# Optimization experiments

Hardware: AMD Instinct MI355X
Metric: run time of the kernel (lower is better)

## Reference

```python
import jax, jax.numpy as jnp
import numpy as np

PAD = 0
SOS = 1
NEG = -1e9


def _lstm_scan(x, Wih, Whh, b, h0, c0, reverse=False):
    # x: [T, B, in]; torch gate order i, f, g, o
    def step(carry, xt):
        h, c = carry
        g = xt @ Wih.T + h @ Whh.T + b
        i, f, gg, o = jnp.split(g, 4, axis=-1)
        c = jax.nn.sigmoid(f) * c + jax.nn.sigmoid(i) * jnp.tanh(gg)
        h = jax.nn.sigmoid(o) * jnp.tanh(c)
        return (h, c), h
    (hT, cT), hs = jax.lax.scan(step, (h0, c0), x, reverse=reverse)
    return hs, hT, cT


def setup_inputs() -> dict:
    B, Ts, Tt = 32, 64, 66
    E, H, V = 512, 512, 16000
    key = jax.random.key(0)
    ks = jax.random.split(key, 16)
    s = 0.05
    n = lambda k, shape: (jax.random.normal(k, shape, dtype=jnp.float32) * s)
    return {
        'src_sentences': jax.random.randint(ks[0], (B, Ts), 4, V),
        'trg_sentences': jax.random.randint(ks[1], (B, Tt), 4, V),
        'src_emb': n(ks[2], (V, E)),
        'trg_emb': n(ks[3], (V, E)),
        'enc0_Wih': n(ks[4], (2, 4 * H, E)),
        'enc0_Whh': n(ks[5], (2, 4 * H, H)),
        'enc0_b': n(ks[6], (2, 4 * H)),
        'enc1_Wih': n(ks[7], (2, 4 * H, 2 * H)),
        'enc1_Whh': n(ks[8], (2, 4 * H, H)),
        'enc1_b': n(ks[9], (2, 4 * H)),
        'dec_Wih': n(ks[10], (8 * H, E)),      # LSTMCell: hidden = 2H -> 4*(2H) gates
        'dec_Whh': n(ks[11], (8 * H, 2 * H)),
        'dec_b': n(ks[12], (8 * H)),
        'out_W1': n(ks[13], (H, 4 * H)),
        'out_W2': n(ks[14], (V - 4, H)),
    }


def reference(src_sentences, trg_sentences, src_emb, trg_emb,
              enc0_Wih, enc0_Whh, enc0_b, enc1_Wih, enc1_Whh, enc1_b,
              dec_Wih, dec_Whh, dec_b, out_W1, out_W2):
    B, Ts = src_sentences.shape
    Tt = trg_sentences.shape[1]
    H = out_W1.shape[0]
    dt = src_emb.dtype
    enc_mask = src_sentences == PAD            # [B, Ts] (all False here)

    # ---- encoder: 2-layer bidirectional LSTM (dropout inactive / eval) ----
    x = jnp.swapaxes(src_emb[src_sentences], 0, 1)   # [Ts, B, E]
    z = jnp.zeros((B, H), dt)
    hf0, hfT, cfT = _lstm_scan(x, enc0_Wih[0], enc0_Whh[0], enc0_b[0], z, z)
    hb0, hbT, cbT = _lstm_scan(x, enc0_Wih[1], enc0_Whh[1], enc0_b[1], z, z, reverse=True)
    x1 = jnp.concatenate([hf0, hb0], axis=-1)        # [Ts, B, 2H]
    hf1, _, _ = _lstm_scan(x1, enc1_Wih[0], enc1_Whh[0], enc1_b[0], z, z)
    hb1, _, _ = _lstm_scan(x1, enc1_Wih[1], enc1_Whh[1], enc1_b[1], z, z, reverse=True)
    enc_out = jnp.swapaxes(jnp.concatenate([hf1, hb1], axis=-1), 0, 1)  # [B, Ts, 2H]
    # module uses encoder_hidden_t[0], [1] -> layer-0 fwd/bwd final states
    hidden = jnp.concatenate([hfT, hbT], axis=-1)    # [B, 2H]
    cell = jnp.concatenate([cfT, cbT], axis=-1)

    # ---- decoder: teacher_force = 1.0 (deterministic) ----
    steps = Tt - 2
    emb_in = jnp.swapaxes(trg_emb[trg_sentences[:, :steps]], 0, 1)  # [steps, B, E]
    tgts = jnp.swapaxes(trg_sentences[:, 1:steps + 1], 0, 1)        # [steps, B]

    def step(carry, inp):
        h, c, loss = carry
        xt, tgt = inp
        g = xt @ dec_Wih.T + h @ dec_Whh.T + dec_b
        i, f, gg, o = jnp.split(g, 4, axis=-1)
        c = jax.nn.sigmoid(f) * c + jax.nn.sigmoid(i) * jnp.tanh(gg)
        h = jax.nn.sigmoid(o) * jnp.tanh(c)
        dmask = tgt == PAD
        h = jnp.where(dmask[:, None], jnp.zeros((), dt), h)  # decoder_hidden_t[mask] = 0
        # dot attention over encoder states
        scores = jnp.einsum('btd,bd->bt', enc_out, h)
        scores = jnp.where(enc_mask, NEG, scores)
        attn = jax.nn.softmax(scores, axis=1)
        ctx = jnp.einsum('bt,btd->bd', attn, enc_out)
        zt = jnp.tanh(jnp.concatenate([h, ctx], axis=-1) @ out_W1.T)
        logits = zt @ out_W2.T                                # [B, V-4]
        logp = jax.nn.log_softmax(logits, axis=1)
        tgt_idx = tgt - 4
        valid = tgt_idx != -4                                 # ignore_index=-4 (PAD)
        safe = jnp.where(valid, tgt_idx, 0)
        nll = -jnp.take_along_axis(logp, safe[:, None], axis=1)[:, 0]
        loss = loss + jnp.sum(jnp.where(valid, nll, jnp.zeros((), dt)))
        pred = jnp.argmax(logits, axis=1) + 4
        return (h, c, loss), pred

    (_, _, loss), preds = jax.lax.scan(step, (hidden, cell, jnp.zeros((), dt)), (emb_in, tgts))
    denom = jnp.sum(trg_sentences[:, 1:-1] != PAD).astype(dt)
    return loss / denom, preds.T  # preds: [B, steps]
```

## Files before the change

### kernel.cpp

```cpp
#include <hip/hip_runtime.h>
#include <hip/hip_bf16.h>
#include <math.h>

#define TSRC 64
#define TTRG 66
#define NVOC 15996
#define NTILE 125

__device__ __forceinline__ float sigm(float x){ return 1.f/(1.f+expf(-x)); }

__global__ __launch_bounds__(256)
void k_gemm128(const float* __restrict__ A, int lda,
               const float* __restrict__ Bw, int ldb,
               const float* __restrict__ bias,
               float* __restrict__ C, int ldc, int K, int nNb)
{
  const int tid = threadIdx.x;
  const int mb = blockIdx.x / nNb;
  const int nb = blockIdx.x % nNb;
  const int m0 = mb*128, n0 = nb*128;

  __shared__ alignas(16) float As[16][132];
  __shared__ alignas(16) float Bs[16][132];
  const int tx = tid & 15;
  const int ty = tid >> 4;
  float acc[8][8];
  #pragma unroll
  for (int i=0;i<8;i++)
    #pragma unroll
    for (int j=0;j<8;j++) acc[i][j]=0.f;

  for (int kt=0; kt<K; kt+=16) {
    #pragma unroll
    for (int i=tid; i<128*16; i+=256) {
      int m = i>>4, k = i&15;
      As[k][m] = A[(size_t)(m0+m)*lda + kt + k];
    }
    #pragma unroll
    for (int i=tid; i<128*16; i+=256) {
      int n = i>>4, k = i&15;
      Bs[k][n] = Bw[(size_t)(n0+n)*ldb + kt + k];
    }
    __syncthreads();
    #pragma unroll
    for (int k=0;k<16;k++) {
      float4 a0 = *reinterpret_cast<const float4*>(&As[k][ty*4]);
      float4 a1 = *reinterpret_cast<const float4*>(&As[k][64+ty*4]);
      float4 b0 = *reinterpret_cast<const float4*>(&Bs[k][tx*4]);
      float4 b1 = *reinterpret_cast<const float4*>(&Bs[k][64+tx*4]);
      float av[8] = {a0.x,a0.y,a0.z,a0.w,a1.x,a1.y,a1.z,a1.w};
      float bv[8] = {b0.x,b0.y,b0.z,b0.w,b1.x,b1.y,b1.z,b1.w};
      #pragma unroll
      for (int i=0;i<8;i++)
        #pragma unroll
        for (int j=0;j<8;j++)
          acc[i][j] = fmaf(av[i], bv[j], acc[i][j]);
    }
    __syncthreads();
  }
  #pragma unroll
  for (int i=0;i<8;i++) {
    int m = m0 + ((i<4) ? ty*4+i : 64+ty*4+(i-4));
    int nA = n0 + tx*4, nB = n0 + 64 + tx*4;
    float4 v0, v1;
    v0.x = acc[i][0] + (bias?bias[nA+0]:0.f);
    v0.y = acc[i][1] + (bias?bias[nA+1]:0.f);
    v0.z = acc[i][2] + (bias?bias[nA+2]:0.f);
    v0.w = acc[i][3] + (bias?bias[nA+3]:0.f);
    v1.x = acc[i][4] + (bias?bias[nB+0]:0.f);
    v1.y = acc[i][5] + (bias?bias[nB+1]:0.f);
    v1.z = acc[i][6] + (bias?bias[nB+2]:0.f);
    v1.w = acc[i][7] + (bias?bias[nB+3]:0.f);
    *reinterpret_cast<float4*>(&C[(size_t)m*ldc + nA]) = v0;
    *reinterpret_cast<float4*>(&C[(size_t)m*ldc + nB]) = v1;
  }
}

__global__ __launch_bounds__(256)
void k_logits(const float* __restrict__ A, const float* __restrict__ Bw,
              const int* __restrict__ trg,
              float* __restrict__ Pmax, int* __restrict__ Parg,
              float* __restrict__ Psum, float* __restrict__ Ltgt)
{
  const int tid = threadIdx.x;
  const int j8   = blockIdx.x & 7;
  const int mb   = (blockIdx.x >> 3) & 15;
  const int nb   = ((blockIdx.x >> 7) << 3) + j8;
  if (nb >= NTILE) return;
  const int m0 = mb*128, n0 = nb*128;

  __shared__ alignas(16) float As[16][132];
  __shared__ alignas(16) float Bs[16][132];
  const int tx = tid & 15;
  const int ty = tid >> 4;
  float acc[8][8];
  #pragma unroll
  for (int i=0;i<8;i++)
    #pragma unroll
    for (int j=0;j<8;j++) acc[i][j]=0.f;

  for (int kt=0; kt<512; kt+=16) {
    #pragma unroll
    for (int i=tid; i<128*16; i+=256) {
      int m = i>>4, k = i&15;
      As[k][m] = A[(size_t)(m0+m)*512 + kt + k];
    }
    #pragma unroll
    for (int i=tid; i<128*16; i+=256) {
      int n = i>>4, k = i&15;
      int gn = n0+n;
      Bs[k][n] = (gn < NVOC) ? Bw[(size_t)gn*512 + kt + k] : 0.f;
    }
    __syncthreads();
    #pragma unroll
    for (int k=0;k<16;k++) {
      float4 a0 = *reinterpret_cast<const float4*>(&As[k][ty*4]);
      float4 a1 = *reinterpret_cast<const float4*>(&As[k][64+ty*4]);
      float4 b0 = *reinterpret_cast<const float4*>(&Bs[k][tx*4]);
      float4 b1 = *reinterpret_cast<const float4*>(&Bs[k][64+tx*4]);
      float av[8] = {a0.x,a0.y,a0.z,a0.w,a1.x,a1.y,a1.z,a1.w};
      float bv[8] = {b0.x,b0.y,b0.z,b0.w,b1.x,b1.y,b1.z,b1.w};
      #pragma unroll
      for (int i=0;i<8;i++)
        #pragma unroll
        for (int j=0;j<8;j++)
          acc[i][j] = fmaf(av[i], bv[j], acc[i][j]);
    }
    __syncthreads();
  }

  #pragma unroll
  for (int i=0;i<8;i++) {
    int r = m0 + ((i<4) ? ty*4+i : 64+ty*4+(i-4));
    int step = r >> 5, b = r & 31;
    int tgt = trg[b*TTRG + step + 1];
    int ti = tgt - 4;
    float m = -3.4e38f; int am = 0x7fffffff;
    #pragma unroll
    for (int j=0;j<8;j++) {
      int gn = n0 + ((j<4) ? tx*4+j : 64+tx*4+(j-4));
      if (gn < NVOC) {
        float x = acc[i][j];
        if (x > m || (x == m && gn < am)) { m = x; am = gn; }
      }
    }
    float s = 0.f;
    float lt = 0.f;
    #pragma unroll
    for (int j=0;j<8;j++) {
      int gn = n0 + ((j<4) ? tx*4+j : 64+tx*4+(j-4));
      if (gn < NVOC) {
        s += expf(acc[i][j] - m);
        if (gn == ti) lt = acc[i][j];
      }
    }
    #pragma unroll
    for (int d=1; d<16; d<<=1) {
      float m2 = __shfl_xor(m, d);
      int   a2 = __shfl_xor(am, d);
      float s2 = __shfl_xor(s, d);
      float l2 = __shfl_xor(lt, d);
      float M = fmaxf(m, m2);
      s = s*expf(m - M) + s2*expf(m2 - M);
      if (m2 > m || (m2 == m && a2 < am)) am = a2;
      m = M;
      lt += l2;
    }
    if (tx == 0) {
      size_t pi = (size_t)r*NTILE + nb;
      Pmax[pi] = m; Parg[pi] = am; Psum[pi] = s;
      if (ti >= n0 && ti < n0 + 128) Ltgt[r] = lt;
    }
  }
}

struct GArgs {
  const float* A;  int lda;
  const float* Bw; int ldb;
  const float* bias;
  float* C; int ldc;
  int N; int K; int nNb; int act;
};

template<int BM,int BN,int BK,int TM,int TN>
__global__ __launch_bounds__(256)
void k_gemm(GArgs a)
{
  const int tid = threadIdx.x;
  const int mb = blockIdx.x / a.nNb;
  const int nb = blockIdx.x % a.nNb;
  const int m0 = mb*BM, n0 = nb*BN;
  const float* A  = a.A + (size_t)m0*a.lda;
  const float* Bw = a.Bw;

  __shared__ float As[BK][BM+1];
  __shared__ float Bs[BK][BN+4];
  const int tx = tid % (BN/TN);
  const int ty = tid / (BN/TN);
  float acc[TM][TN];
  #pragma unroll
  for (int i=0;i<TM;i++)
    #pragma unroll
    for (int j=0;j<TN;j++) acc[i][j]=0.f;

  for (int kt=0; kt<a.K; kt+=BK) {
    #pragma unroll
    for (int i=tid; i<BM*BK; i+=256) {
      int m = i/BK, k = i%BK;
      As[k][m] = A[(size_t)m*a.lda + kt + k];
    }
    #pragma unroll
    for (int i=tid; i<BN*BK; i+=256) {
      int n = i/BK, k = i%BK;
      int gn = n0+n;
      Bs[k][n] = (gn < a.N) ? Bw[(size_t)gn*a.ldb + kt + k] : 0.f;
    }
    __syncthreads();
    #pragma unroll
    for (int k=0;k<BK;k++) {
      float av[TM], bv[TN];
      #pragma unroll
      for (int i=0;i<TM;i++) av[i]=As[k][ty*TM+i];
      #pragma unroll
      for (int j=0;j<TN;j++) bv[j]=Bs[k][tx*TN+j];
      #pragma unroll
      for (int i=0;i<TM;i++)
        #pragma unroll
        for (int j=0;j<TN;j++)
          acc[i][j] = fmaf(av[i], bv[j], acc[i][j]);
    }
    __syncthreads();
  }
  #pragma unroll
  for (int i=0;i<TM;i++) {
    int m = m0 + ty*TM + i;
    #pragma unroll
    for (int j=0;j<TN;j++) {
      int n = n0 + tx*TN + j;
      if (n < a.N) {
        float v = acc[i][j];
        if (a.bias) v += a.bias[n];
        if (a.act)  v = tanhf(v);
        a.C[(size_t)m*a.ldc + n] = v;
      }
    }
  }
}

__global__ __launch_bounds__(128)
void k_combine(const float* __restrict__ Pmax, const int* __restrict__ Parg,
               const float* __restrict__ Psum, const float* __restrict__ Ltgt,
               const int* __restrict__ trg,
               float* __restrict__ nll, float* __restrict__ outp)
{
  int r = blockIdx.x;
  int step = r >> 5, b = r & 31;
  int tid = threadIdx.x;
  __shared__ float sm[128]; __shared__ int sa[128]; __shared__ float ssum[128];
  float m = -3.4e38f; int am = 0x7fffffff; float s = 0.f;
  if (tid < NTILE) {
    size_t pi = (size_t)r*NTILE + tid;
    m = Pmax[pi]; am = Parg[pi]; s = Psum[pi];
  }
  sm[tid]=m; sa[tid]=am; ssum[tid]=s; __syncthreads();
  for (int off=64; off; off>>=1) {
    if (tid < off) {
      float m2 = sm[tid+off]; int a2 = sa[tid+off]; float s2 = ssum[tid+off];
      float m1 = sm[tid];     int a1 = sa[tid];     float s1 = ssum[tid];
      float M = fmaxf(m1, m2);
      ssum[tid] = s1*expf(m1 - M) + s2*expf(m2 - M);
      if (m2 > m1 || (m2 == m1 && a2 < a1)) sa[tid] = a2;
      sm[tid] = M;
    }
    __syncthreads();
  }
  if (tid == 0) {
    int tgt = trg[b*TTRG + step + 1];
    float nl = 0.f;
    if (tgt != 0) nl = -(Ltgt[r] - sm[0] - logf(ssum[0]));
    nll[step*32 + b] = nl;
    outp[1 + b*64 + step] = (float)(sa[0] + 4);
  }
}

__global__ void k_gather(const float* __restrict__ emb, const int* __restrict__ tok,
                         float* __restrict__ outp, int Tfull)
{
  int r = blockIdx.x;
  int t = r >> 5, b = r & 31;
  int token = tok[b*Tfull + t];
  const float4* s = (const float4*)(emb + (size_t)token*512);
  float4* d = (float4*)(outp + (size_t)r*512);
  d[threadIdx.x] = s[threadIdx.x];
}

__global__ __launch_bounds__(256)
void k_estep(const float* __restrict__ Whh,
             const float* __restrict__ xg,
             const float* __restrict__ hin,
             float* __restrict__ hout,
             float* __restrict__ cst,
             float* __restrict__ xout, int s)
{
  const int bid = blockIdx.x;
  const int dir = bid >> 7;
  const int j0  = (bid & 127) * 4;
  const int tid = threadIdx.x;
  const int kg  = tid >> 5;
  const int b   = tid & 31;
  __shared__ float4 wl4[16*128];
  __shared__ float red[4*16*33];

  {
    const float* W = Whh + (size_t)dir*2048*512;
    for (int idx = tid; idx < 16*128; idx += 256) {
      int r = idx >> 7, c = idx & 127;
      int g = r >> 2, jj = r & 3;
      wl4[idx] = ((const float4*)(W + (size_t)(g*512 + j0 + jj)*512))[c];
    }
  }
  float4 hreg[16];
  {
    const float4* H4 = (const float4*)(hin + (size_t)dir*32*512);
    #pragma unroll
    for (int j=0;j<16;j++) hreg[j] = H4[(size_t)b*128 + kg*16 + j];
  }
  __syncthreads();

  float acc[16];
  #pragma unroll
  for (int r=0;r<16;r++) {
    const float4* wr = wl4 + r*128 + kg*16;
    float a0=0.f,a1=0.f,a2=0.f,a3=0.f;
    #pragma unroll
    for (int j=0;j<16;j++) {
      float4 w = wr[j];
      a0 = fmaf(w.x, hreg[j].x, a0);
      a1 = fmaf(w.y, hreg[j].y, a1);
      a2 = fmaf(w.z, hreg[j].z, a2);
      a3 = fmaf(w.w, hreg[j].w, a3);
    }
    acc[r] = (a0+a1)+(a2+a3);
  }
  #pragma unroll
  for (int r=0;r<16;r++) acc[r] += __shfl_xor(acc[r], 32);
  const int wv = tid >> 6;
  if ((tid & 32) == 0) {
    #pragma unroll
    for (int r=0;r<16;r++) red[wv*528 + r*33 + b] = acc[r];
  }
  __syncthreads();

  if (tid < 128) {
    int jj = tid >> 5, bb = tid & 31;
    int jh = j0 + jj;
    int t  = dir ? (63 - s) : s;
    const float* x = xg + ((size_t)t*32 + bb)*4096 + dir*2048;
    float g4[4];
    #pragma unroll
    for (int g=0; g<4; g++) {
      int r = g*4 + jj;
      g4[g] = ((red[0*528 + r*33 + bb] + red[1*528 + r*33 + bb])
             + (red[2*528 + r*33 + bb] + red[3*528 + r*33 + bb]))
             + x[g*512 + jh];
    }
    size_t ci = ((size_t)dir*32 + bb)*512 + jh;
    float cn = sigm(g4[1])*cst[ci] + sigm(g4[0])*tanhf(g4[2]);
    float hn = sigm(g4[3])*tanhf(cn);
    cst[ci] = cn;
    hout[ci] = hn;
    xout[((size_t)t*32 + bb)*1024 + dir*512 + jh] = hn;
  }
}

__global__ __launch_bounds__(256, 2)
void k_mstep(const float* __restrict__ eWhh,
             const float* __restrict__ exg,
             const float* __restrict__ ehin, float* __restrict__ ehout,
             float* __restrict__ ecst,
             float* __restrict__ encout,
             const float* __restrict__ dWih,
             const float* __restrict__ dWhh,
             const float* __restrict__ db,
             const float* __restrict__ xemb,
             const float* __restrict__ dhin,
             float* __restrict__ dcst,
             float* __restrict__ dhall_t,
             const int* __restrict__ trg, int s)
{
  const int tid = threadIdx.x;
  const int kg  = tid >> 5;
  const int b   = tid & 31;
  __shared__ float4 wl4[16*256];
  __shared__ float red[4*16*33];

  float acc[16];

  if (blockIdx.x < 256) {
    const int dir = blockIdx.x >> 7;
    const int j0  = (blockIdx.x & 127) * 4;
    {
      const float* W = eWhh + (size_t)dir*2048*512;
      for (int idx = tid; idx < 16*128; idx += 256) {
        int r = idx >> 7, c = idx & 127;
        int g = r >> 2, jj = r & 3;
        wl4[idx] = ((const float4*)(W + (size_t)(g*512 + j0 + jj)*512))[c];
      }
    }
    float4 hreg[16];
    {
      const float4* H4 = (const float4*)(ehin + (size_t)dir*32*512);
      #pragma unroll
      for (int j=0;j<16;j++) hreg[j] = H4[(size_t)b*128 + kg*16 + j];
    }
    __syncthreads();
    #pragma unroll
    for (int r=0;r<16;r++) {
      const float4* wr = wl4 + r*128 + kg*16;
      float a0=0.f,a1=0.f,a2=0.f,a3=0.f;
      #pragma unroll
      for (int j=0;j<16;j++) {
        float4 w = wr[j];
        a0 = fmaf(w.x, hreg[j].x, a0);
        a1 = fmaf(w.y, hreg[j].y, a1);
        a2 = fmaf(w.z, hreg[j].z, a2);
        a3 = fmaf(w.w, hreg[j].w, a3);
      }
      acc[r] = (a0+a1)+(a2+a3);
    }
    #pragma unroll
    for (int r=0;r<16;r++) acc[r] += __shfl_xor(acc[r], 32);
    const int wv = tid >> 6;
    if ((tid & 32) == 0) {
      #pragma unroll
      for (int r=0;r<16;r++) red[wv*528 + r*33 + b] = acc[r];
    }
    __syncthreads();
    if (tid < 128) {
      int jj = tid >> 5, bb = tid & 31;
      int jh = j0 + jj;
      int t  = dir ? (63 - s) : s;
      const float* x = exg + ((size_t)t*32 + bb)*4096 + dir*2048;
      float g4[4];
      #pragma unroll
      for (int g=0; g<4; g++) {
        int r = g*4 + jj;
        g4[g] = ((red[0*528 + r*33 + bb] + red[1*528 + r*33 + bb])
               + (red[2*528 + r*33 + bb] + red[3*528 + r*33 + bb]))
               + x[g*512 + jh];
      }
      size_t ci = ((size_t)dir*32 + bb)*512 + jh;
      float cn = sigm(g4[1])*ecst[ci] + sigm(g4[0])*tanhf(g4[2]);
      float hn = sigm(g4[3])*tanhf(cn);
      ecst[ci] = cn;
      ehout[ci] = hn;
      encout[((size_t)bb*64 + t)*1024 + dir*512 + jh] = hn;
    }
  } else {
    const int j0 = (blockIdx.x - 256) * 4;
    for (int idx = tid; idx < 16*128; idx += 256) {
      int r = idx >> 7, c = idx & 127;
      int g = r >> 2, jj = r & 3;
      wl4[idx] = ((const float4*)(dWih + (size_t)(g*1024 + j0 + jj)*512))[c];
    }
    {
      float4 xreg[16];
      const float4* X4 = (const float4*)(xemb + (size_t)s*32*512);
      #pragma unroll
      for (int j=0;j<16;j++) xreg[j] = X4[(size_t)b*128 + kg*16 + j];
      __syncthreads();
      #pragma unroll
      for (int r=0;r<16;r++) {
        const float4* wr = wl4 + r*128 + kg*16;
        float a0=0.f,a1=0.f,a2=0.f,a3=0.f;
        #pragma unroll
        for (int j=0;j<16;j++) {
          float4 w = wr[j];
          a0 = fmaf(w.x, xreg[j].x, a0);
          a1 = fmaf(w.y, xreg[j].y, a1);
          a2 = fmaf(w.z, xreg[j].z, a2);
          a3 = fmaf(w.w, xreg[j].w, a3);
        }
        acc[r] = (a0+a1)+(a2+a3);
      }
    }
    __syncthreads();
    for (int idx = tid; idx < 16*256; idx += 256) {
      int r = idx >> 8, c = idx & 255;
      int g = r >> 2, jj = r & 3;
      wl4[idx] = ((const float4*)(dWhh + (size_t)(g*1024 + j0 + jj)*1024))[c];
    }
    __syncthreads();
    #pragma unroll
    for (int kh=0; kh<2; kh++) {
      float4 hreg[16];
      const float4* H4 = (const float4*)dhin;
      #pragma unroll
      for (int j=0;j<16;j++) hreg[j] = H4[(size_t)b*256 + kg*32 + kh*16 + j];
      #pragma unroll
      for (int r=0;r<16;r++) {
        const float4* wr = wl4 + r*256 + kg*32 + kh*16;
        float a0=0.f,a1=0.f,a2=0.f,a3=0.f;
        #pragma unroll
        for (int j=0;j<16;j++) {
          float4 w = wr[j];
          a0 = fmaf(w.x, hreg[j].x, a0);
          a1 = fmaf(w.y, hreg[j].y, a1);
          a2 = fmaf(w.z, hreg[j].z, a2);
          a3 = fmaf(w.w, hreg[j].w, a3);
        }
        acc[r] += (a0+a1)+(a2+a3);
      }
    }
    #pragma unroll
    for (int r=0;r<16;r++) acc[r] += __shfl_xor(acc[r], 32);
    const int wv = tid >> 6;
    if ((tid & 32) == 0) {
      #pragma unroll
      for (int r=0;r<16;r++) red[wv*528 + r*33 + b] = acc[r];
    }
    __syncthreads();
    if (tid < 128) {
      int jj = tid >> 5, bb = tid & 31;
      int jh = j0 + jj;
      int tgt = trg[bb*TTRG + s + 1];
      bool dm = (tgt == 0);
      float g4[4];
      #pragma unroll
      for (int g=0; g<4; g++) {
        int r = g*4 + jj;
        g4[g] = ((red[0*528 + r*33 + bb] + red[1*528 + r*33 + bb])
               + (red[2*528 + r*33 + bb] + red[3*528 + r*33 + bb]))
               + db[g*1024 + jh];
      }
      size_t ci = (size_t)bb*1024 + jh;
      float cn = sigm(g4[1])*dcst[ci] + sigm(g4[0])*tanhf(g4[2]);
      float hn = sigm(g4[3])*tanhf(cn);
      dcst[ci] = cn;
      dhall_t[ci] = dm ? 0.f : hn;
    }
  }
}

__global__ void k_pack(const float* __restrict__ hfin, const float* __restrict__ cfin,
                       float* __restrict__ dh, float* __restrict__ dcc)
{
  int tid = blockIdx.x*256 + threadIdx.x;
  int j = tid & 1023, b = tid >> 10;
  int dir = j >> 9, jj = j & 511;
  size_t si = ((size_t)dir*32 + b)*512 + jj;
  dh[(size_t)b*1024 + j]  = hfin[si];
  dcc[(size_t)b*1024 + j] = cfin[si];
}

__global__ __launch_bounds__(256)
void k_attn(const float* __restrict__ Hall,
            const float* __restrict__ encout,
            const int* __restrict__ src,
            float* __restrict__ hctx)
{
  int bid = blockIdx.x;
  int t = bid >> 5, b = bid & 31;
  int tid = threadIdx.x;
  __shared__ float sh[1024];
  __shared__ float ssc[64];
  const float* h = Hall + ((size_t)t*32 + b)*1024;
  size_t row = (size_t)t*32 + b;
  #pragma unroll
  for (int r=0;r<4;r++) {
    int jh = tid + 256*r;
    float v = h[jh];
    sh[jh] = v;
    hctx[row*2048 + jh] = v;
  }
  __syncthreads();
  {
    int tq = tid >> 2, part = tid & 3;
    const float* eo = encout + ((size_t)b*64 + tq)*1024 + part*256;
    const float* hh = sh + part*256;
    float s = 0.f;
    for (int k=0;k<256;k++) s = fmaf(hh[k], eo[k], s);
    s += __shfl_xor(s, 1);
    s += __shfl_xor(s, 2);
    if (part == 0) ssc[tq] = (src[b*TSRC + tq] == 0) ? -1e9f : s;
  }
  __syncthreads();
  if (tid < 64) {
    float v = ssc[tid];
    float m = v;
    for (int d=1; d<64; d<<=1) m = fmaxf(m, __shfl_xor(m, d));
    float e = expf(v - m);
    float su = e;
    for (int d=1; d<64; d<<=1) su += __shfl_xor(su, d);
    ssc[tid] = e / su;
  }
  __syncthreads();
  #pragma unroll
  for (int r=0;r<4;r++) {
    int k = tid + 256*r;
    float a = 0.f;
    const float* eb = encout + (size_t)b*65536 + k;
    for (int tt=0;tt<64;tt++) a = fmaf(ssc[tt], eb[tt*1024], a);
    hctx[row*2048 + 1024 + k] = a;
  }
}

__global__ __launch_bounds__(256)
void k_final(const float* __restrict__ nll, const int* __restrict__ trg,
             float* __restrict__ outp)
{
  int tid = threadIdx.x;
  __shared__ float ss[256]; __shared__ int sc[256];
  float s = 0.f; int cnt = 0;
  for (int i=tid; i<2048; i+=256) {
    s += nll[i];
    int b = i >> 6, t = (i & 63) + 1;
    cnt += (trg[b*TTRG + t] != 0);
  }
  ss[tid]=s; sc[tid]=cnt; __syncthreads();
  for (int off=128; off; off>>=1) {
    if (tid<off) { ss[tid]+=ss[tid+off]; sc[tid]+=sc[tid+off]; }
    __syncthreads();
  }
  if (tid==0) outp[0] = ss[0] / (float)sc[0];
}

static void launch_big(hipStream_t st, const float* A, int lda,
                       const float* Bw, int ldb, const float* bias,
                       float* C, int ldc, int M, int N, int K)
{
  int nNb = N/128;
  dim3 g((M/128)*nNb, 1, 1);
  k_gemm128<<<g, dim3(256), 0, st>>>(A, lda, Bw, ldb, bias, C, ldc, K, nNb);
}

static void launch_med(hipStream_t st, const float* A, int lda,
                       const float* Bw, int ldb, const float* bias,
                       float* C, int ldc, int M, int N, int K, int act)
{
  GArgs a;
  a.A=A; a.lda=lda;
  a.Bw=Bw; a.ldb=ldb;
  a.bias=bias;
  a.C=C; a.ldc=ldc;
  a.N=N; a.K=K; a.nNb=(N+63)/64; a.act=act;
  dim3 g((M/64)*a.nNb, 1, 1);
  k_gemm<64,64,16,4,4><<<g, dim3(256), 0, st>>>(a);
}

extern "C" void kernel_launch(void* const* d_in, const int* in_sizes, int n_in,
                              void* d_out, int out_size, void* d_ws, size_t ws_size,
                              hipStream_t stream)
{
  (void)in_sizes; (void)n_in; (void)out_size; (void)ws_size;
  const int*   src   = (const int*)  d_in[0];
  const int*   trg   = (const int*)  d_in[1];
  const float* semb  = (const float*)d_in[2];
  const float* temb  = (const float*)d_in[3];
  const float* e0Wih = (const float*)d_in[4];
  const float* e0Whh = (const float*)d_in[5];
  const float* e0b   = (const float*)d_in[6];
  const float* e1Wih = (const float*)d_in[7];
  const float* e1Whh = (const float*)d_in[8];
  const float* e1b   = (const float*)d_in[9];
  const float* dWih  = (const float*)d_in[10];
  const float* dWhh  = (const float*)d_in[11];
  const float* db    = (const float*)d_in[12];
  const float* W1    = (const float*)d_in[13];
  const float* W2    = (const float*)d_in[14];
  float* out = (float*)d_out;

  float* ws = (float*)d_ws;
  size_t o = 0;
  float* x_in   = ws + o; o += (size_t)2048*512;
  float* xg     = ws + o; o += (size_t)2048*4096;
  float* x1     = ws + o; o += (size_t)2048*1024;
  float* encout = ws + o; o += (size_t)2048*1024;
  float* hA     = ws + o; o += 2*32*512;
  float* hB     = ws + o; o += 2*32*512;
  float* cbuf   = ws + o; o += 2*32*512;
  float* dh0    = ws + o; o += 32*1024;
  float* dc     = ws + o; o += 32*1024;
  float* nll    = ws + o; o += 2048;
  float* Hall   = x1;
  float* hctx   = xg;
  float* zt     = x_in;
  float* Pmax   = xg + (size_t)4*1024*1024;
  int*   Parg   = (int*)(Pmax + (size_t)2048*NTILE);
  float* Psum   = Pmax + (size_t)2*2048*NTILE;
  float* Ltgt   = Pmax + (size_t)3*2048*NTILE;

  hipMemsetAsync(hA,   0, 2*32*512*sizeof(float), stream);
  hipMemsetAsync(cbuf, 0, 2*32*512*sizeof(float), stream);
  k_gather<<<dim3(2048), dim3(128), 0, stream>>>(semb, src, x_in, TSRC);
  launch_big(stream, x_in, 512, e0Wih, 512, e0b, xg, 4096, 2048, 4096, 512);
  for (int s=0; s<64; s++) {
    float* hin  = (s&1) ? hB : hA;
    float* hout = (s&1) ? hA : hB;
    k_estep<<<dim3(256), dim3(256), 0, stream>>>(e0Whh, xg, hin, hout, cbuf, x1, s);
  }
  k_pack<<<dim3(128), dim3(256), 0, stream>>>(hA, cbuf, dh0, dc);

  hipMemsetAsync(hA,   0, 2*32*512*sizeof(float), stream);
  hipMemsetAsync(cbuf, 0, 2*32*512*sizeof(float), stream);
  launch_big(stream, x1, 1024, e1Wih, 1024, e1b, xg, 4096, 2048, 4096, 1024);
  k_gather<<<dim3(2048), dim3(128), 0, stream>>>(temb, trg, x_in, TTRG);

  for (int s=0; s<64; s++) {
    float* ehin  = (s&1) ? hB : hA;
    float* ehout = (s&1) ? hA : hB;
    const float* dhin = (s == 0) ? dh0 : (Hall + (size_t)(s-1)*32*1024);
    k_mstep<<<dim3(512), dim3(256), 0, stream>>>(
        e1Whh, xg, ehin, ehout, cbuf, encout,
        dWih, dWhh, db, x_in, dhin, dc, Hall + (size_t)s*32*1024, trg, s);
  }

  k_attn<<<dim3(2048), dim3(256), 0, stream>>>(Hall, encout, src, hctx);
  launch_med(stream, hctx, 2048, W1, 2048, nullptr, zt, 512, 2048, 512, 2048, 1);
  k_logits<<<dim3(2048), dim3(256), 0, stream>>>(zt, W2, trg, Pmax, Parg, Psum, Ltgt);
  k_combine<<<dim3(2048), dim3(128), 0, stream>>>(Pmax, Parg, Psum, Ltgt, trg, nll, out);
  k_final<<<dim3(1), dim3(256), 0, stream>>>(nll, trg, out);
}
```

Baseline: 4.078 ms.

## Fuse LSTM input projections and embedding gathers into per-step recurrent kernels

Drops the upfront batched input-projection GEMMs and embedding gather kernels for both encoder layers and the decoder input. Each recurrent step kernel now loads its slice of the input weights and computes the input-gate contribution itself, reading embeddings by token id or the previous layer's output directly. This removes several kernel launches and the large xg intermediate buffer. In exchange, every one of the sequential steps must also stream the input-weight slices (twice the hidden width for layer 1), which puts that work on the serial critical path. The decoder history buffer is moved into the xg region because x1 is now still needed during the second loop.

Result: slower. 4.340 ms (+6.4%).

```diff
diff --git a/kernel.cpp b/kernel.cpp
--- a/kernel.cpp
+++ b/kernel.cpp
@@ -8,73 +8,6 @@
 #define NTILE 125
 
 __device__ __forceinline__ float sigm(float x){ return 1.f/(1.f+expf(-x)); }
-
-__global__ __launch_bounds__(256)
-void k_gemm128(const float* __restrict__ A, int lda,
-               const float* __restrict__ Bw, int ldb,
-               const float* __restrict__ bias,
-               float* __restrict__ C, int ldc, int K, int nNb)
-{
-  const int tid = threadIdx.x;
-  const int mb = blockIdx.x / nNb;
-  const int nb = blockIdx.x % nNb;
-  const int m0 = mb*128, n0 = nb*128;
-
-  __shared__ alignas(16) float As[16][132];
-  __shared__ alignas(16) float Bs[16][132];
-  const int tx = tid & 15;
-  const int ty = tid >> 4;
-  float acc[8][8];
-  #pragma unroll
-  for (int i=0;i<8;i++)
-    #pragma unroll
-    for (int j=0;j<8;j++) acc[i][j]=0.f;
-
-  for (int kt=0; kt<K; kt+=16) {
-    #pragma unroll
-    for (int i=tid; i<128*16; i+=256) {
-      int m = i>>4, k = i&15;
-      As[k][m] = A[(size_t)(m0+m)*lda + kt + k];
-    }
-    #pragma unroll
-    for (int i=tid; i<128*16; i+=256) {
-      int n = i>>4, k = i&15;
-      Bs[k][n] = Bw[(size_t)(n0+n)*ldb + kt + k];
-    }
-    __syncthreads();
-    #pragma unroll
-    for (int k=0;k<16;k++) {
-      float4 a0 = *reinterpret_cast<const float4*>(&As[k][ty*4]);
-      float4 a1 = *reinterpret_cast<const float4*>(&As[k][64+ty*4]);
-      float4 b0 = *reinterpret_cast<const float4*>(&Bs[k][tx*4]);
-      float4 b1 = *reinterpret_cast<const float4*>(&Bs[k][64+tx*4]);
-      float av[8] = {a0.x,a0.y,a0.z,a0.w,a1.x,a1.y,a1.z,a1.w};
-      float bv[8] = {b0.x,b0.y,b0.z,b0.w,b1.x,b1.y,b1.z,b1.w};
-      #pragma unroll
-      for (int i=0;i<8;i++)
-        #pragma unroll
-        for (int j=0;j<8;j++)
-          acc[i][j] = fmaf(av[i], bv[j], acc[i][j]);
-    }
-    __syncthreads();
-  }
-  #pragma unroll
-  for (int i=0;i<8;i++) {
-    int m = m0 + ((i<4) ? ty*4+i : 64+ty*4+(i-4));
-    int nA = n0 + tx*4, nB = n0 + 64 + tx*4;
-    float4 v0, v1;
-    v0.x = acc[i][0] + (bias?bias[nA+0]:0.f);
-    v0.y = acc[i][1] + (bias?bias[nA+1]:0.f);
-    v0.z = acc[i][2] + (bias?bias[nA+2]:0.f);
-    v0.w = acc[i][3] + (bias?bias[nA+3]:0.f);
-    v1.x = acc[i][4] + (bias?bias[nB+0]:0.f);
-    v1.y = acc[i][5] + (bias?bias[nB+1]:0.f);
-    v1.z = acc[i][6] + (bias?bias[nB+2]:0.f);
-    v1.w = acc[i][7] + (bias?bias[nB+3]:0.f);
-    *reinterpret_cast<float4*>(&C[(size_t)m*ldc + nA]) = v0;
-    *reinterpret_cast<float4*>(&C[(size_t)m*ldc + nB]) = v1;
-  }
-}
 
 __global__ __launch_bounds__(256)
 void k_logits(const float* __restrict__ A, const float* __restrict__ Bw,
@@ -283,24 +216,17 @@
   }
 }
 
-__global__ void k_gather(const float* __restrict__ emb, const int* __restrict__ tok,
-                         float* __restrict__ outp, int Tfull)
-{
-  int r = blockIdx.x;
-  int t = r >> 5, b = r & 31;
-  int token = tok[b*Tfull + t];
-  const float4* s = (const float4*)(emb + (size_t)token*512);
-  float4* d = (float4*)(outp + (size_t)r*512);
-  d[threadIdx.x] = s[threadIdx.x];
-}
-
 __global__ __launch_bounds__(256)
-void k_estep(const float* __restrict__ Whh,
-             const float* __restrict__ xg,
+void k_estep(const float* __restrict__ Wih,
+             const float* __restrict__ Whh,
+             const float* __restrict__ bias2,
+             const float* __restrict__ emb,
+             const int* __restrict__ toks,
              const float* __restrict__ hin,
              float* __restrict__ hout,
              float* __restrict__ cst,
-             float* __restrict__ xout, int s)
+             float* __restrict__ xout,
+             int s)
 {
   const int bid = blockIdx.x;
   const int dir = bid >> 7;
@@ -310,37 +236,64 @@
   const int b   = tid & 31;
   __shared__ float4 wl4[16*128];
   __shared__ float red[4*16*33];
-
+  const int t = dir ? (63 - s) : s;
+  float acc[16];
+
+  for (int idx = tid; idx < 16*128; idx += 256) {
+    int r = idx >> 7, c = idx & 127;
+    int g = r >> 2, jj = r & 3;
+    wl4[idx] = ((const float4*)(Wih + (size_t)dir*2048*512
+                                + (size_t)(g*512 + j0 + jj)*512))[c];
+  }
   {
-    const float* W = Whh + (size_t)dir*2048*512;
-    for (int idx = tid; idx < 16*128; idx += 256) {
-      int r = idx >> 7, c = idx & 127;
-      int g = r >> 2, jj = r & 3;
-      wl4[idx] = ((const float4*)(W + (size_t)(g*512 + j0 + jj)*512))[c];
-    }
-  }
-  float4 hreg[16];
+    float4 xreg[16];
+    int tok = toks[b*TSRC + t];
+    const float4* X4 = (const float4*)(emb + (size_t)tok*512);
+    #pragma unroll
+    for (int j=0;j<16;j++) xreg[j] = X4[kg*16 + j];
+    __syncthreads();
+    #pragma unroll
+    for (int r=0;r<16;r++) {
+      const float4* wr = wl4 + r*128 + kg*16;
+      float a0=0.f,a1=0.f,a2=0.f,a3=0.f;
+      #pragma unroll
+      for (int j=0;j<16;j++) {
+        float4 w = wr[j];
+        a0 = fmaf(w.x, xreg[j].x, a0);
+        a1 = fmaf(w.y, xreg[j].y, a1);
+        a2 = fmaf(w.z, xreg[j].z, a2);
+        a3 = fmaf(w.w, xreg[j].w, a3);
+      }
+      acc[r] = (a0+a1)+(a2+a3);
+    }
+  }
+  __syncthreads();
+  for (int idx = tid; idx < 16*128; idx += 256) {
+    int r = idx >> 7, c = idx & 127;
+    int g = r >> 2, jj = r & 3;
+    wl4[idx] = ((const float4*)(Whh + (size_t)dir*2048*512
+                                + (size_t)(g*512 + j0 + jj)*512))[c];
+  }
   {
+    float4 hreg[16];
     const float4* H4 = (const float4*)(hin + (size_t)dir*32*512);
     #pragma unroll
     for (int j=0;j<16;j++) hreg[j] = H4[(size_t)b*128 + kg*16 + j];
-  }
-  __syncthreads();
-
-  float acc[16];
-  #pragma unroll
-  for (int r=0;r<16;r++) {
-    const float4* wr = wl4 + r*128 + kg*16;
-    float a0=0.f,a1=0.f,a2=0.f,a3=0.f;
-    #pragma unroll
-    for (int j=0;j<16;j++) {
-      float4 w = wr[j];
-      a0 = fmaf(w.x, hreg[j].x, a0);
-      a1 = fmaf(w.y, hreg[j].y, a1);
-      a2 = fmaf(w.z, hreg[j].z, a2);
-      a3 = fmaf(w.w, hreg[j].w, a3);
-    }
-    acc[r] = (a0+a1)+(a2+a3);
+    __syncthreads();
+    #pragma unroll
+    for (int r=0;r<16;r++) {
+      const float4* wr = wl4 + r*128 + kg*16;
+      float a0=0.f,a1=0.f,a2=0.f,a3=0.f;
+      #pragma unroll
+      for (int j=0;j<16;j++) {
+        float4 w = wr[j];
+        a0 = fmaf(w.x, hreg[j].x, a0);
+        a1 = fmaf(w.y, hreg[j].y, a1);
+        a2 = fmaf(w.z, hreg[j].z, a2);
+        a3 = fmaf(w.w, hreg[j].w, a3);
+      }
+      acc[r] += (a0+a1)+(a2+a3);
+    }
   }
   #pragma unroll
   for (int r=0;r<16;r++) acc[r] += __shfl_xor(acc[r], 32);
@@ -354,15 +307,13 @@
   if (tid < 128) {
     int jj = tid >> 5, bb = tid & 31;
     int jh = j0 + jj;
-    int t  = dir ? (63 - s) : s;
-    const float* x = xg + ((size_t)t*32 + bb)*4096 + dir*2048;
     float g4[4];
     #pragma unroll
     for (int g=0; g<4; g++) {
       int r = g*4 + jj;
       g4[g] = ((red[0*528 + r*33 + bb] + red[1*528 + r*33 + bb])
              + (red[2*528 + r*33 + bb] + red[3*528 + r*33 + bb]))
-             + x[g*512 + jh];
+             + bias2[dir*2048 + g*512 + jh];
     }
     size_t ci = ((size_t)dir*32 + bb)*512 + jh;
     float cn = sigm(g4[1])*cst[ci] + sigm(g4[0])*tanhf(g4[2]);
@@ -374,19 +325,22 @@
 }
 
 __global__ __launch_bounds__(256, 2)
-void k_mstep(const float* __restrict__ eWhh,
-             const float* __restrict__ exg,
+void k_mstep(const float* __restrict__ eWih,
+             const float* __restrict__ eWhh,
+             const float* __restrict__ eb2,
+             const float* __restrict__ x1,
              const float* __restrict__ ehin, float* __restrict__ ehout,
              float* __restrict__ ecst,
              float* __restrict__ encout,
              const float* __restrict__ dWih,
              const float* __restrict__ dWhh,
              const float* __restrict__ db,
-             const float* __restrict__ xemb,
+             const float* __restrict__ temb,
+             const int* __restrict__ trg,
              const float* __restrict__ dhin,
              float* __restrict__ dcst,
              float* __restrict__ dhall_t,
-             const int* __restrict__ trg, int s)
+             int s)
 {
   const int tid = threadIdx.x;
   const int kg  = tid >> 5;
@@ -399,34 +353,63 @@
   if (blockIdx.x < 256) {
     const int dir = blockIdx.x >> 7;
     const int j0  = (blockIdx.x & 127) * 4;
-    {
-      const float* W = eWhh + (size_t)dir*2048*512;
+    const int t   = dir ? (63 - s) : s;
+    #pragma unroll
+    for (int kh=0; kh<2; kh++) {
       for (int idx = tid; idx < 16*128; idx += 256) {
         int r = idx >> 7, c = idx & 127;
         int g = r >> 2, jj = r & 3;
-        wl4[idx] = ((const float4*)(W + (size_t)(g*512 + j0 + jj)*512))[c];
-      }
-    }
-    float4 hreg[16];
+        wl4[idx] = ((const float4*)(eWih + (size_t)dir*2048*1024
+                    + (size_t)(g*512 + j0 + jj)*1024 + (size_t)kh*512))[c];
+      }
+      float4 xreg[16];
+      const float4* X4 = (const float4*)(x1 + ((size_t)t*32 + b)*1024);
+      #pragma unroll
+      for (int j=0;j<16;j++) xreg[j] = X4[kh*128 + kg*16 + j];
+      __syncthreads();
+      #pragma unroll
+      for (int r=0;r<16;r++) {
+        const float4* wr = wl4 + r*128 + kg*16;
+        float a0=0.f,a1=0.f,a2=0.f,a3=0.f;
+        #pragma unroll
+        for (int j=0;j<16;j++) {
+          float4 w = wr[j];
+          a0 = fmaf(w.x, xreg[j].x, a0);
+          a1 = fmaf(w.y, xreg[j].y, a1);
+          a2 = fmaf(w.z, xreg[j].z, a2);
+          a3 = fmaf(w.w, xreg[j].w, a3);
+        }
+        float sum = (a0+a1)+(a2+a3);
+        acc[r] = (kh == 0) ? sum : (acc[r] + sum);
+      }
+      __syncthreads();
+    }
+    for (int idx = tid; idx < 16*128; idx += 256) {
+      int r = idx >> 7, c = idx & 127;
+      int g = r >> 2, jj = r & 3;
+      wl4[idx] = ((const float4*)(eWhh + (size_t)dir*2048*512
+                  + (size_t)(g*512 + j0 + jj)*512))[c];
+    }
     {
+      float4 hreg[16];
       const float4* H4 = (const float4*)(ehin + (size_t)dir*32*512);
       #pragma unroll
       for (int j=0;j<16;j++) hreg[j] = H4[(size_t)b*128 + kg*16 + j];
-    }
-    __syncthreads();
-    #pragma unroll
-    for (int r=0;r<16;r++) {
-      const float4* wr = wl4 + r*128 + kg*16;
-      float a0=0.f,a1=0.f,a2=0.f,a3=0.f;
-      #pragma unroll
-      for (int j=0;j<16;j++) {
-        float4 w = wr[j];
-        a0 = fmaf(w.x, hreg[j].x, a0);
-        a1 = fmaf(w.y, hreg[j].y, a1);
-        a2 = fmaf(w.z, hreg[j].z, a2);
-        a3 = fmaf(w.w, hreg[j].w, a3);
-      }
-      acc[r] = (a0+a1)+(a2+a3);
+      __syncthreads();
+      #pragma unroll
+      for (int r=0;r<16;r++) {
+        const float4* wr = wl4 + r*128 + kg*16;
+        float a0=0.f,a1=0.f,a2=0.f,a3=0.f;
+        #pragma unroll
+        for (int j=0;j<16;j++) {
+          float4 w = wr[j];
+          a0 = fmaf(w.x, hreg[j].x, a0);
+          a1 = fmaf(w.y, hreg[j].y, a1);
+          a2 = fmaf(w.z, hreg[j].z, a2);
+          a3 = fmaf(w.w, hreg[j].w, a3);
+        }
+        acc[r] += (a0+a1)+(a2+a3);
+      }
     }
     #pragma unroll
     for (int r=0;r<16;r++) acc[r] += __shfl_xor(acc[r], 32);
@@ -439,15 +422,13 @@
     if (tid < 128) {
       int jj = tid >> 5, bb = tid & 31;
       int jh = j0 + jj;
-      int t  = dir ? (63 - s) : s;
-      const float* x = exg + ((size_t)t*32 + bb)*4096 + dir*2048;
       float g4[4];
       #pragma unroll
       for (int g=0; g<4; g++) {
         int r = g*4 + jj;
         g4[g] = ((red[0*528 + r*33 + bb] + red[1*528 + r*33 + bb])
                + (red[2*528 + r*33 + bb] + red[3*528 + r*33 + bb]))
-               + x[g*512 + jh];
+               + eb2[dir*2048 + g*512 + jh];
       }
       size_t ci = ((size_t)dir*32 + bb)*512 + jh;
       float cn = sigm(g4[1])*ecst[ci] + sigm(g4[0])*tanhf(g4[2]);
@@ -465,9 +446,10 @@
     }
     {
       float4 xreg[16];
-      const float4* X4 = (const float4*)(xemb + (size_t)s*32*512);
-      #pragma unroll
-      for (int j=0;j<16;j++) xreg[j] = X4[(size_t)b*128 + kg*16 + j];
+      int tok = trg[b*TTRG + s];
+      const float4* X4 = (const float4*)(temb + (size_t)tok*512);
+      #pragma unroll
+      for (int j=0;j<16;j++) xreg[j] = X4[kg*16 + j];
       __syncthreads();
       #pragma unroll
       for (int r=0;r<16;r++) {
@@ -623,15 +605,6 @@
     __syncthreads();
   }
   if (tid==0) outp[0] = ss[0] / (float)sc[0];
-}
-
-static void launch_big(hipStream_t st, const float* A, int lda,
-                       const float* Bw, int ldb, const float* bias,
-                       float* C, int ldc, int M, int N, int K)
-{
-  int nNb = N/128;
-  dim3 g((M/128)*nNb, 1, 1);
-  k_gemm128<<<g, dim3(256), 0, st>>>(A, lda, Bw, ldb, bias, C, ldc, K, nNb);
 }
 
 static void launch_med(hipStream_t st, const float* A, int lda,
@@ -682,37 +655,33 @@
   float* dh0    = ws + o; o += 32*1024;
   float* dc     = ws + o; o += 32*1024;
   float* nll    = ws + o; o += 2048;
-  float* Hall   = x1;
   float* hctx   = xg;
-  float* zt     = x_in;
   float* Pmax   = xg + (size_t)4*1024*1024;
   int*   Parg   = (int*)(Pmax + (size_t)2048*NTILE);
   float* Psum   = Pmax + (size_t)2*2048*NTILE;
   float* Ltgt   = Pmax + (size_t)3*2048*NTILE;
+  float* Hall   = xg + (size_t)5*1024*1024;
+  float* zt     = x_in;
 
   hipMemsetAsync(hA,   0, 2*32*512*sizeof(float), stream);
   hipMemsetAsync(cbuf, 0, 2*32*512*sizeof(float), stream);
-  k_gather<<<dim3(2048), dim3(128), 0, stream>>>(semb, src, x_in, TSRC);
-  launch_big(stream, x_in, 512, e0Wih, 512, e0b, xg, 4096, 2048, 4096, 512);
   for (int s=0; s<64; s++) {
     float* hin  = (s&1) ? hB : hA;
     float* hout = (s&1) ? hA : hB;
-    k_estep<<<dim3(256), dim3(256), 0, stream>>>(e0Whh, xg, hin, hout, cbuf, x1, s);
+    k_estep<<<dim3(256), dim3(256), 0, stream>>>(e0Wih, e0Whh, e0b, semb, src,
+                                                 hin, hout, cbuf, x1, s);
   }
   k_pack<<<dim3(128), dim3(256), 0, stream>>>(hA, cbuf, dh0, dc);
 
   hipMemsetAsync(hA,   0, 2*32*512*sizeof(float), stream);
   hipMemsetAsync(cbuf, 0, 2*32*512*sizeof(float), stream);
-  launch_big(stream, x1, 1024, e1Wih, 1024, e1b, xg, 4096, 2048, 4096, 1024);
-  k_gather<<<dim3(2048), dim3(128), 0, stream>>>(temb, trg, x_in, TTRG);
-
   for (int s=0; s<64; s++) {
     float* ehin  = (s&1) ? hB : hA;
     float* ehout = (s&1) ? hA : hB;
     const float* dhin = (s == 0) ? dh0 : (Hall + (size_t)(s-1)*32*1024);
     k_mstep<<<dim3(512), dim3(256), 0, stream>>>(
-        e1Whh, xg, ehin, ehout, cbuf, encout,
-        dWih, dWhh, db, x_in, dhin, dc, Hall + (size_t)s*32*1024, trg, s);
+        e1Wih, e1Whh, e1b, x1, ehin, ehout, cbuf, encout,
+        dWih, dWhh, db, temb, trg, dhin, dc, Hall + (size_t)s*32*1024, s);
   }
 
   k_attn<<<dim3(2048), dim3(256), 0, stream>>>(Hall, encout, src, hctx);
```
